# Optimization experiments

Hardware: AMD Instinct MI355X
Metric: run time of the kernel (lower is better)

The kernel has to match this reference:

```python
import jax, jax.numpy as jnp
import numpy as np


def _edt(mask):
    """Exact 2D Euclidean distance transform: distance from each pixel to the
    nearest foreground (mask==1) pixel. Matches scipy distance_transform_edt(1-mask).
    mask: [B, H, W] float32 in {0,1}. Returns [B, H, W] float32 distances.
    Samples with no foreground return all-zeros (matching the torch module).
    """
    b, h, w = mask.shape
    big = jnp.float32(h + w)  # > max possible distance sqrt(h^2+w^2)
    rows = jnp.arange(h, dtype=jnp.float32)[None, :, None]  # [1,H,1]
    fg = mask > 0
    # Phase 1: per-column 1D distance along the row axis.
    last = jax.lax.cummax(jnp.where(fg, rows, -big), axis=1)              # nearest fg row above
    nxt = jax.lax.cummin(jnp.where(fg, rows, 3.0 * big), axis=1, reverse=True)  # nearest fg row below
    g = jnp.minimum(jnp.minimum(rows - last, nxt - rows), big)            # [B,H,W]
    # Phase 2: for each row, D[x] = min_j (x-j)^2 + g[j]^2 (exact, brute-force min).
    cols = jnp.arange(w, dtype=jnp.float32)
    diff2 = (cols[:, None] - cols[None, :]) ** 2                          # [W,W]
    g2 = g * g                                                            # [B,H,W]
    dist2 = jnp.min(diff2[None, None, :, :] + g2[:, :, None, :], axis=-1)  # [B,H,W]
    dist = jnp.sqrt(dist2)
    has_fg = jnp.any(fg, axis=(1, 2))                                     # [B]
    return jnp.where(has_fg[:, None, None], dist, 0.0)


def setup_inputs() -> dict:
    key = jax.random.key(0)
    k1, k2 = jax.random.split(key)
    pred = jax.random.normal(k1, (4, 1, 512, 512), dtype=jnp.float32)
    target = jax.random.randint(k2, (4, 1, 512, 512), 0, 2, dtype=jnp.int32)
    return {"pred": pred, "target": target}


def reference(pred, target):
    # pred: [B,1,H,W] logits; target: [B,1,H,W] binary (int)
    p = jax.nn.sigmoid(pred)
    dist_map = _edt(target[:, 0].astype(jnp.float32))[:, None]  # [B,1,H,W]
    return jnp.mean(p * dist_map)
```

## Files before the change

kernel.cpp:

```cpp
#include <hip/hip_runtime.h>
#include <math.h>

#define BH 4
#define HH 512
#define WW 512
#define NPIX (BH * HH * WW)
#define NTILES 8
#define NSEG 16
#define SEGROWS 32


__global__ __launch_bounds__(1024) void edt_col_scan(
    const int* __restrict__ tgt, float* __restrict__ g2,
    int* __restrict__ blockAny) {
    const int b    = blockIdx.x >> 3;
    const int xt   = blockIdx.x & 7;
    const int lane = threadIdx.x & 63;
    const int wave = threadIdx.x >> 6;
    const int x    = xt * 64 + lane;
    const int y0   = wave * SEGROWS;
    const int* t   = tgt + b * HH * WW + x;
    float* gp      = g2  + b * HH * WW + x;

    int v[SEGROWS];
    #pragma unroll
    for (int i = 0; i < SEGROWS; ++i)
        v[i] = t[(y0 + i) * WW];

    int segLast = -1024, segFirst = 3 * 1024;
    #pragma unroll
    for (int i = 0; i < SEGROWS; ++i)
        if (v[i] > 0) segLast = y0 + i;
    #pragma unroll
    for (int i = SEGROWS - 1; i >= 0; --i)
        if (v[i] > 0) segFirst = y0 + i;

    __shared__ int sLast[NSEG][64];
    __shared__ int sFirst[NSEG][64];
    __shared__ int sAny[NSEG];
    sLast[wave][lane]  = segLast;
    sFirst[wave][lane] = segFirst;
    unsigned long long bal = __ballot(segLast >= 0);
    if (lane == 0) sAny[wave] = (bal != 0ull);
    __syncthreads();

    int carryLast = -1024;
    for (int s = 0; s < wave; ++s)
        carryLast = max(carryLast, sLast[s][lane]);
    int carryFirst = 3 * 1024;
    for (int s = wave + 1; s < NSEG; ++s)
        carryFirst = min(carryFirst, sFirst[s][lane]);

    int gup[SEGROWS];
    int last = carryLast;
    #pragma unroll
    for (int i = 0; i < SEGROWS; ++i) {
        int y = y0 + i;
        if (v[i] > 0) last = y;
        gup[i] = y - last;
    }
    int nxt = carryFirst;
    #pragma unroll
    for (int i = SEGROWS - 1; i >= 0; --i) {
        int y = y0 + i;
        if (v[i] > 0) nxt = y;
        int g = min(min(gup[i], nxt - y), 1024);
        float gf = (float)g;
        gp[y * WW] = gf * gf;
    }

    if (threadIdx.x == 0) {
        int a = 0;
        #pragma unroll
        for (int s = 0; s < NSEG; ++s) a |= sAny[s];
        blockAny[blockIdx.x] = a;
    }
}

__global__ __launch_bounds__(256) void edt_row_loss(
    const float* __restrict__ pred, const float* __restrict__ g2,
    float* __restrict__ rowSum) {
    const int row  = blockIdx.x;
    const int base = row * WW;
    const int tid  = threadIdx.x;

    __shared__ float sg2[WW];
    sg2[tid]       = g2[base + tid];
    sg2[tid + 256] = g2[base + tid + 256];
    __syncthreads();

    float acc = 0.0f;
    #pragma unroll
    for (int k = 0; k < 2; ++k) {
        const int x = tid + k * 256;
        float m = sg2[x];
        for (int r = 1; r < WW; ++r) {
            float r2 = (float)(r * r);
            if (r2 >= m) break;
            int jl = x - r, jr = x + r;
            if (jl >= 0) m = fminf(m, sg2[jl] + r2);
            if (jr < WW) m = fminf(m, sg2[jr] + r2);
            if (jl < 0 && jr >= WW) break;
        }
        float p = 1.0f / (1.0f + expf(-pred[base + x]));
        acc += p * sqrtf(m);
    }

    #pragma unroll
    for (int off = 32; off > 0; off >>= 1)
        acc += __shfl_down(acc, off);
    __shared__ float sw[4];
    if ((tid & 63) == 0) sw[tid >> 6] = acc;
    __syncthreads();
    if (tid == 0) rowSum[row] = sw[0] + sw[1] + sw[2] + sw[3];
}

__global__ __launch_bounds__(256) void finalize(
    const float* __restrict__ rowSum, const int* __restrict__ blockAny,
    float* __restrict__ out) {
    const int tid = threadIdx.x;
    __shared__ float sflag[BH];
    if (tid < BH) {
        int a = 0;
        #pragma unroll
        for (int i = 0; i < NTILES; ++i) a |= blockAny[tid * NTILES + i];
        sflag[tid] = a ? 1.0f : 0.0f;
    }
    __syncthreads();
    float acc = 0.0f;
    for (int i = tid; i < BH * HH; i += 256)
        acc += rowSum[i] * sflag[i >> 9];
    #pragma unroll
    for (int off = 32; off > 0; off >>= 1)
        acc += __shfl_down(acc, off);
    __shared__ float sw[4];
    if ((tid & 63) == 0) sw[tid >> 6] = acc;
    __syncthreads();
    if (tid == 0) out[0] = (sw[0] + sw[1] + sw[2] + sw[3]) * (1.0f / (float)NPIX);
}

extern "C" void kernel_launch(void* const* d_in, const int* in_sizes, int n_in,
                              void* d_out, int out_size, void* d_ws, size_t ws_size,
                              hipStream_t stream) {
    const float* pred = (const float*)d_in[0];
    const int* tgt    = (const int*)d_in[1];
    float* out        = (float*)d_out;

    char* ws        = (char*)d_ws;
    int* blockAny   = (int*)ws;
    float* rowSum   = (float*)(ws + 128);
    float* g2       = (float*)(ws + 16384);

    edt_col_scan<<<BH * NTILES, 1024, 0, stream>>>(tgt, g2, blockAny);
    edt_row_loss<<<BH * HH, 256, 0, stream>>>(pred, g2, rowSum);
    finalize<<<1, 256, 0, stream>>>(rowSum, blockAny, out);
}
```

Measured before the change: 70.30 us.

## Fold finalize into row kernel via atomic ticket and reshape column scan blocks

```diff
diff --git a/kernel.cpp b/kernel.cpp
--- a/kernel.cpp
+++ b/kernel.cpp
@@ -5,22 +5,25 @@
 #define HH 512
 #define WW 512
 #define NPIX (BH * HH * WW)
-#define NTILES 8
+#define CPB 32
+#define NXT (WW / CPB)
 #define NSEG 16
 #define SEGROWS 32
 
 
-__global__ __launch_bounds__(1024) void edt_col_scan(
+__global__ __launch_bounds__(512) void edt_col_scan(
     const int* __restrict__ tgt, float* __restrict__ g2,
-    int* __restrict__ blockAny) {
-    const int b    = blockIdx.x >> 3;
-    const int xt   = blockIdx.x & 7;
-    const int lane = threadIdx.x & 63;
-    const int wave = threadIdx.x >> 6;
-    const int x    = xt * 64 + lane;
-    const int y0   = wave * SEGROWS;
-    const int* t   = tgt + b * HH * WW + x;
-    float* gp      = g2  + b * HH * WW + x;
+    int* __restrict__ blockAny, int* __restrict__ ticket) {
+    const int b   = blockIdx.x >> 4;
+    const int xt  = blockIdx.x & 15;
+    const int col = threadIdx.x & (CPB - 1);
+    const int seg = threadIdx.x >> 5;
+    const int x   = xt * CPB + col;
+    const int y0  = seg * SEGROWS;
+    const int* t  = tgt + b * HH * WW + x;
+    float* gp     = g2  + b * HH * WW + x;
+
+    if (blockIdx.x == 0 && threadIdx.x == 0) *ticket = 0;
 
     int v[SEGROWS];
     #pragma unroll
@@ -35,21 +38,24 @@
     for (int i = SEGROWS - 1; i >= 0; --i)
         if (v[i] > 0) segFirst = y0 + i;
 
-    __shared__ int sLast[NSEG][64];
-    __shared__ int sFirst[NSEG][64];
-    __shared__ int sAny[NSEG];
-    sLast[wave][lane]  = segLast;
-    sFirst[wave][lane] = segFirst;
-    unsigned long long bal = __ballot(segLast >= 0);
-    if (lane == 0) sAny[wave] = (bal != 0ull);
+    __shared__ int sLast[NSEG][CPB];
+    __shared__ int sFirst[NSEG][CPB];
+    sLast[seg][col]  = segLast;
+    sFirst[seg][col] = segFirst;
     __syncthreads();
 
     int carryLast = -1024;
-    for (int s = 0; s < wave; ++s)
-        carryLast = max(carryLast, sLast[s][lane]);
+    #pragma unroll
+    for (int s = 0; s < NSEG; ++s)
+        if (s < seg) carryLast = max(carryLast, sLast[s][col]);
     int carryFirst = 3 * 1024;
-    for (int s = wave + 1; s < NSEG; ++s)
-        carryFirst = min(carryFirst, sFirst[s][lane]);
+    #pragma unroll
+    for (int s = 0; s < NSEG; ++s)
+        if (s > seg) carryFirst = min(carryFirst, sFirst[s][col]);
+
+    int fullLast = max(carryLast, segLast);
+    unsigned long long bal = __ballot(seg == NSEG - 1 && fullLast >= 0);
+    if (threadIdx.x == 512 - CPB) blockAny[blockIdx.x] = (bal != 0ull) ? 1 : 0;
 
     int gup[SEGROWS];
     int last = carryLast;
@@ -68,25 +74,22 @@
         float gf = (float)g;
         gp[y * WW] = gf * gf;
     }
-
-    if (threadIdx.x == 0) {
-        int a = 0;
-        #pragma unroll
-        for (int s = 0; s < NSEG; ++s) a |= sAny[s];
-        blockAny[blockIdx.x] = a;
-    }
 }
 
 __global__ __launch_bounds__(256) void edt_row_loss(
     const float* __restrict__ pred, const float* __restrict__ g2,
-    float* __restrict__ rowSum) {
+    float* __restrict__ rowSum, const int* __restrict__ blockAny,
+    int* __restrict__ ticket, float* __restrict__ out) {
     const int row  = blockIdx.x;
     const int base = row * WW;
     const int tid  = threadIdx.x;
 
+    float pr0 = pred[base + tid];
+    float pr1 = pred[base + tid + 256];
+
     __shared__ float sg2[WW];
-    sg2[tid]       = g2[base + tid];
-    sg2[tid + 256] = g2[base + tid + 256];
+    float2 gv = ((const float2*)(g2 + base))[tid];
+    ((float2*)sg2)[tid] = gv;
     __syncthreads();
 
     float acc = 0.0f;
@@ -102,7 +105,7 @@
             if (jr < WW) m = fminf(m, sg2[jr] + r2);
             if (jl < 0 && jr >= WW) break;
         }
-        float p = 1.0f / (1.0f + expf(-pred[base + x]));
+        float p = 1.0f / (1.0f + __expf(-(k == 0 ? pr0 : pr1)));
         acc += p * sqrtf(m);
     }
 
@@ -113,30 +116,33 @@
     if ((tid & 63) == 0) sw[tid >> 6] = acc;
     __syncthreads();
     if (tid == 0) rowSum[row] = sw[0] + sw[1] + sw[2] + sw[3];
-}
 
-__global__ __launch_bounds__(256) void finalize(
-    const float* __restrict__ rowSum, const int* __restrict__ blockAny,
-    float* __restrict__ out) {
-    const int tid = threadIdx.x;
-    __shared__ float sflag[BH];
-    if (tid < BH) {
-        int a = 0;
+    __threadfence();
+    __shared__ int isLast;
+    if (tid == 0) isLast = (atomicAdd(ticket, 1) == BH * HH - 1) ? 1 : 0;
+    __syncthreads();
+    if (isLast) {
+        __threadfence();
+        __shared__ float sflag[BH];
+        if (tid < BH) {
+            int a = 0;
+            #pragma unroll
+            for (int i = 0; i < NXT; ++i) a |= blockAny[tid * NXT + i];
+            sflag[tid] = a ? 1.0f : 0.0f;
+        }
+        __syncthreads();
+        float facc = 0.0f;
+        for (int i = tid; i < BH * HH; i += 256)
+            facc += rowSum[i] * sflag[i >> 9];
         #pragma unroll
-        for (int i = 0; i < NTILES; ++i) a |= blockAny[tid * NTILES + i];
-        sflag[tid] = a ? 1.0f : 0.0f;
+        for (int off = 32; off > 0; off >>= 1)
+            facc += __shfl_down(facc, off);
+        __shared__ float fsw[4];
+        if ((tid & 63) == 0) fsw[tid >> 6] = facc;
+        __syncthreads();
+        if (tid == 0)
+            out[0] = (fsw[0] + fsw[1] + fsw[2] + fsw[3]) * (1.0f / (float)NPIX);
     }
-    __syncthreads();
-    float acc = 0.0f;
-    for (int i = tid; i < BH * HH; i += 256)
-        acc += rowSum[i] * sflag[i >> 9];
-    #pragma unroll
-    for (int off = 32; off > 0; off >>= 1)
-        acc += __shfl_down(acc, off);
-    __shared__ float sw[4];
-    if ((tid & 63) == 0) sw[tid >> 6] = acc;
-    __syncthreads();
-    if (tid == 0) out[0] = (sw[0] + sw[1] + sw[2] + sw[3]) * (1.0f / (float)NPIX);
 }
 
 extern "C" void kernel_launch(void* const* d_in, const int* in_sizes, int n_in,
@@ -146,12 +152,12 @@
     const int* tgt    = (const int*)d_in[1];
     float* out        = (float*)d_out;
 
-    char* ws        = (char*)d_ws;
-    int* blockAny   = (int*)ws;
-    float* rowSum   = (float*)(ws + 128);
-    float* g2       = (float*)(ws + 16384);
+    char* ws      = (char*)d_ws;
+    int* blockAny = (int*)ws;
+    int* ticket   = (int*)(ws + 256);
+    float* rowSum = (float*)(ws + 512);
+    float* g2     = (float*)(ws + 16384);
 
-    edt_col_scan<<<BH * NTILES, 1024, 0, stream>>>(tgt, g2, blockAny);
-    edt_row_loss<<<BH * HH, 256, 0, stream>>>(pred, g2, rowSum);
-    finalize<<<1, 256, 0, stream>>>(rowSum, blockAny, out);
+    edt_col_scan<<<BH * NXT, 512, 0, stream>>>(tgt, g2, blockAny, ticket);
+    edt_row_loss<<<BH * HH, 256, 0, stream>>>(pred, g2, rowSum, blockAny, ticket, out);
 }
```

Result: slower. 221.9 us (+215.7%).

## Fuse final reduction into row kernel via atomic ticket, prefetch pred, vectorize g2 load

Applied to the files above, without the earlier changes.

```diff
diff --git a/kernel.cpp b/kernel.cpp
--- a/kernel.cpp
+++ b/kernel.cpp
@@ -12,7 +12,8 @@
 
 __global__ __launch_bounds__(1024) void edt_col_scan(
     const int* __restrict__ tgt, float* __restrict__ g2,
-    int* __restrict__ blockAny) {
+    int* __restrict__ blockAny, int* __restrict__ ticket,
+    float* __restrict__ accum) {
     const int b    = blockIdx.x >> 3;
     const int xt   = blockIdx.x & 7;
     const int lane = threadIdx.x & 63;
@@ -21,6 +22,8 @@
     const int y0   = wave * SEGROWS;
     const int* t   = tgt + b * HH * WW + x;
     float* gp      = g2  + b * HH * WW + x;
+
+    if (blockIdx.x == 0 && threadIdx.x == 0) { *ticket = 0; *accum = 0.0f; }
 
     int v[SEGROWS];
     #pragma unroll
@@ -79,14 +82,18 @@
 
 __global__ __launch_bounds__(256) void edt_row_loss(
     const float* __restrict__ pred, const float* __restrict__ g2,
-    float* __restrict__ rowSum) {
+    const int* __restrict__ blockAny, int* __restrict__ ticket,
+    float* __restrict__ accum, float* __restrict__ out) {
     const int row  = blockIdx.x;
+    const int b    = row >> 9;
     const int base = row * WW;
     const int tid  = threadIdx.x;
 
+    float pr0 = pred[base + tid];
+    float pr1 = pred[base + tid + 256];
+
     __shared__ float sg2[WW];
-    sg2[tid]       = g2[base + tid];
-    sg2[tid + 256] = g2[base + tid + 256];
+    ((float2*)sg2)[tid] = ((const float2*)(g2 + base))[tid];
     __syncthreads();
 
     float acc = 0.0f;
@@ -102,7 +109,7 @@
             if (jr < WW) m = fminf(m, sg2[jr] + r2);
             if (jl < 0 && jr >= WW) break;
         }
-        float p = 1.0f / (1.0f + expf(-pred[base + x]));
+        float p = 1.0f / (1.0f + __expf(-(k == 0 ? pr0 : pr1)));
         acc += p * sqrtf(m);
     }
 
@@ -112,31 +119,22 @@
     __shared__ float sw[4];
     if ((tid & 63) == 0) sw[tid >> 6] = acc;
     __syncthreads();
-    if (tid == 0) rowSum[row] = sw[0] + sw[1] + sw[2] + sw[3];
-}
 
-__global__ __launch_bounds__(256) void finalize(
-    const float* __restrict__ rowSum, const int* __restrict__ blockAny,
-    float* __restrict__ out) {
-    const int tid = threadIdx.x;
-    __shared__ float sflag[BH];
-    if (tid < BH) {
+    if (tid == 0) {
         int a = 0;
         #pragma unroll
-        for (int i = 0; i < NTILES; ++i) a |= blockAny[tid * NTILES + i];
-        sflag[tid] = a ? 1.0f : 0.0f;
+        for (int i = 0; i < NTILES; ++i) a |= blockAny[b * NTILES + i];
+        float val = (sw[0] + sw[1] + sw[2] + sw[3]) *
+                    (a ? 1.0f : 0.0f) * (1.0f / (float)NPIX);
+
+        float old = atomicAdd(accum, val);
+        asm volatile("" :: "v"(old));
+        int t = atomicAdd(ticket, 1);
+        if (t == BH * HH - 1) {
+            float total = atomicAdd(accum, 0.0f);
+            out[0] = total;
+        }
     }
-    __syncthreads();
-    float acc = 0.0f;
-    for (int i = tid; i < BH * HH; i += 256)
-        acc += rowSum[i] * sflag[i >> 9];
-    #pragma unroll
-    for (int off = 32; off > 0; off >>= 1)
-        acc += __shfl_down(acc, off);
-    __shared__ float sw[4];
-    if ((tid & 63) == 0) sw[tid >> 6] = acc;
-    __syncthreads();
-    if (tid == 0) out[0] = (sw[0] + sw[1] + sw[2] + sw[3]) * (1.0f / (float)NPIX);
 }
 
 extern "C" void kernel_launch(void* const* d_in, const int* in_sizes, int n_in,
@@ -146,12 +144,12 @@
     const int* tgt    = (const int*)d_in[1];
     float* out        = (float*)d_out;
 
-    char* ws        = (char*)d_ws;
-    int* blockAny   = (int*)ws;
-    float* rowSum   = (float*)(ws + 128);
-    float* g2       = (float*)(ws + 16384);
+    char* ws      = (char*)d_ws;
+    int* blockAny = (int*)ws;
+    int* ticket   = (int*)(ws + 128);
+    float* accum  = (float*)(ws + 132);
+    float* g2     = (float*)(ws + 16384);
 
-    edt_col_scan<<<BH * NTILES, 1024, 0, stream>>>(tgt, g2, blockAny);
-    edt_row_loss<<<BH * HH, 256, 0, stream>>>(pred, g2, rowSum);
-    finalize<<<1, 256, 0, stream>>>(rowSum, blockAny, out);
+    edt_col_scan<<<BH * NTILES, 1024, 0, stream>>>(tgt, g2, blockAny, ticket, accum);
+    edt_row_loss<<<BH * HH, 256, 0, stream>>>(pred, g2, blockAny, ticket, accum, out);
 }
```

New measurement: 116.3 us. +65.5%, slower.
